# Optimization experiments

Measured on AMD Instinct MI355X. Metric: run time of the kernel, lower is better.

## Reference

```python
import jax, jax.numpy as jnp
import numpy as np

V = 100000   # num nodes
T = 8        # num edge types
E = 400000   # edges per type
D = 128      # node feature dim


def setup_inputs() -> dict:
    key = jax.random.key(0)
    k1, k2, k3 = jax.random.split(key, 3)
    node_values = jax.random.normal(k1, (V, D), dtype=jnp.float32)
    # edges[t, 0] = src indices, edges[t, 1] = dest indices for edge type t
    edges = jax.random.randint(k2, (T, 2, E), 0, V, dtype=jnp.int32)
    W = jax.random.normal(k3, (T * D, D), dtype=jnp.float32) * 0.02
    b = jnp.zeros((D,), dtype=jnp.float32)
    return {"node_values": node_values, "edges": edges, "W": W, "b": b}


def reference(node_values, edges, W, b):
    Vn = node_values.shape[0]

    def per_type(src, dest):
        # norm_weights: sqrt(degree) per node, computed from index occurrence counts
        deg_src = jnp.zeros((Vn,), node_values.dtype).at[src].add(1.0)
        deg_dst = jnp.zeros((Vn,), node_values.dtype).at[dest].add(1.0)
        ns = jnp.sqrt(jnp.maximum(deg_src, 1.0))  # [V]
        nd = jnp.sqrt(jnp.maximum(deg_dst, 1.0))  # [V]
        msg = (node_values / ns[:, None])[src]                      # gather: [E, D]
        agg = jax.ops.segment_sum(msg, dest, num_segments=Vn)       # reduce: [V, D]
        return agg / nd[:, None]

    # vmap over edge types: [T, V, D]
    msgs = jax.vmap(per_type)(edges[:, 0], edges[:, 1])
    # tf.stack(..., axis=1) -> [V, T, D]; reshape to [V, T*D]
    msgs = jnp.transpose(msgs, (1, 0, 2)).reshape(Vn, -1)
    # Dense
    return msgs @ W + b
```

## Files before the change

kernel.cpp:

```cpp
#include <hip/hip_runtime.h>
#include <hip/hip_bf16.h>
#include <stdint.h>

#define NV 100000
#define NT 8
#define NE 400000
#define ND 128
#define NTV (NT * NV)
#define SC1B ((NTV + 1023) / 1024)
#define XCVT ((NV * ND / 8) / 256)

typedef float  f32x4  __attribute__((ext_vector_type(4)));
typedef short  bf16x8 __attribute__((ext_vector_type(8)));

static __device__ __forceinline__ unsigned short f2bf(float f) {
    unsigned u = __float_as_uint(f);
    u += 0x7fffu + ((u >> 16) & 1u);
    return (unsigned short)(u >> 16);
}

__global__ __launch_bounds__(256) void k_count(const int* __restrict__ edges,
                                               unsigned* __restrict__ cs,
                                               unsigned* __restrict__ cd) {
    int i = blockIdx.x * 256 + threadIdx.x;
    if (i >= NT * NE / 4) return;
    int t = i / (NE / 4);
    int e = (i - t * (NE / 4)) * 4;
    const int* base = edges + (size_t)t * 2 * NE;
    int4 s4 = *(const int4*)&base[e];
    int4 d4 = *(const int4*)&base[NE + e];
    unsigned* cst = cs + t * NV;
    unsigned* cdt = cd + t * NV;
    atomicAdd(&cst[s4.x], 1u); atomicAdd(&cst[s4.y], 1u);
    atomicAdd(&cst[s4.z], 1u); atomicAdd(&cst[s4.w], 1u);
    atomicAdd(&cdt[d4.x], 1u); atomicAdd(&cdt[d4.y], 1u);
    atomicAdd(&cdt[d4.z], 1u); atomicAdd(&cdt[d4.w], 1u);
}

__global__ __launch_bounds__(256) void k_scan1(const unsigned* __restrict__ cnt,
                                               unsigned* __restrict__ off,
                                               unsigned* __restrict__ bsum) {
    __shared__ unsigned sm[256];
    int tid  = threadIdx.x;
    int base = blockIdx.x * 1024 + tid * 4;
    unsigned v0 = (base + 0 < NTV) ? cnt[base + 0] : 0u;
    unsigned v1 = (base + 1 < NTV) ? cnt[base + 1] : 0u;
    unsigned v2 = (base + 2 < NTV) ? cnt[base + 2] : 0u;
    unsigned v3 = (base + 3 < NTV) ? cnt[base + 3] : 0u;
    unsigned s4 = v0 + v1 + v2 + v3;
    sm[tid] = s4;
    __syncthreads();
    for (int d = 1; d < 256; d <<= 1) {
        unsigned tv = (tid >= d) ? sm[tid - d] : 0u;
        __syncthreads();
        sm[tid] += tv;
        __syncthreads();
    }
    unsigned excl = sm[tid] - s4;
    if (tid == 255) bsum[blockIdx.x] = sm[255];
    if (base + 0 < NTV) off[base + 0] = excl;
    if (base + 1 < NTV) off[base + 1] = excl + v0;
    if (base + 2 < NTV) off[base + 2] = excl + v0 + v1;
    if (base + 3 < NTV) off[base + 3] = excl + v0 + v1 + v2;
}

__global__ __launch_bounds__(1024) void k_scan2(unsigned* __restrict__ bsum) {
    __shared__ unsigned sm[1024];
    int tid = threadIdx.x;
    unsigned v = (tid < SC1B) ? bsum[tid] : 0u;
    sm[tid] = v;
    __syncthreads();
    for (int d = 1; d < 1024; d <<= 1) {
        unsigned tv = (tid >= d) ? sm[tid - d] : 0u;
        __syncthreads();
        sm[tid] += tv;
        __syncthreads();
    }
    if (tid < SC1B) bsum[tid] = sm[tid] - v;
}

__global__ __launch_bounds__(256) void k_scan3(unsigned* __restrict__ off,
                                               const unsigned* __restrict__ bsum,
                                               unsigned* __restrict__ cursor,
                                               unsigned* __restrict__ cs) {
    int i = blockIdx.x * 256 + threadIdx.x;
    if (i < NTV) {
        unsigned v = off[i] + bsum[i >> 10];
        off[i]    = v;
        cursor[i] = v;
        unsigned a = cs[i];
        ((float*)cs)[i] = rsqrtf((float)(a > 1u ? a : 1u));
    }
    if (i == 0) off[NTV] = (unsigned)(NT * NE);
}

__global__ __launch_bounds__(256) void k_cvt(const float* __restrict__ x,
                                             unsigned short* __restrict__ xb,
                                             const float* __restrict__ W,
                                             unsigned short* __restrict__ Wt) {
    if (blockIdx.x < XCVT) {
        int i = blockIdx.x * 256 + threadIdx.x;
        const float4 a = *(const float4*)&x[(size_t)i * 8];
        const float4 b = *(const float4*)&x[(size_t)i * 8 + 4];
        union { unsigned short us[8]; uint4 v; } pk;
        pk.us[0] = f2bf(a.x); pk.us[1] = f2bf(a.y);
        pk.us[2] = f2bf(a.z); pk.us[3] = f2bf(a.w);
        pk.us[4] = f2bf(b.x); pk.us[5] = f2bf(b.y);
        pk.us[6] = f2bf(b.z); pk.us[7] = f2bf(b.w);
        *(uint4*)&xb[(size_t)i * 8] = pk.v;
    } else {
        int i = (blockIdx.x - XCVT) * 256 + threadIdx.x;
        int t = i >> 14;
        int r = i & 16383;
        int col = r >> 7;
        int k   = r & 127;
        Wt[i] = f2bf(W[((size_t)t * 128 + k) * 128 + col]);
    }
}

__global__ __launch_bounds__(256) void k_fill(const int* __restrict__ edges,
                                              unsigned* __restrict__ cursor,
                                              int* __restrict__ elist) {
    int i = blockIdx.x * 256 + threadIdx.x;
    if (i >= NT * NE / 4) return;
    int t = i / (NE / 4);
    int e = (i - t * (NE / 4)) * 4;
    const int* base = edges + (size_t)t * 2 * NE;
    int4 s4 = *(const int4*)&base[e];
    int4 d4 = *(const int4*)&base[NE + e];
    unsigned* curt = cursor + t * NV;
    unsigned p0 = atomicAdd(&curt[d4.x], 1u); elist[p0] = s4.x;
    unsigned p1 = atomicAdd(&curt[d4.y], 1u); elist[p1] = s4.y;
    unsigned p2 = atomicAdd(&curt[d4.z], 1u); elist[p2] = s4.z;
    unsigned p3 = atomicAdd(&curt[d4.w], 1u); elist[p3] = s4.w;
}

#define ACC8(dst, c, s)                                                      \
    do {                                                                     \
        (dst)[0] = fmaf(__uint_as_float((c).x << 16), (s), (dst)[0]);        \
        (dst)[1] = fmaf(__uint_as_float((c).x & 0xffff0000u), (s), (dst)[1]);\
        (dst)[2] = fmaf(__uint_as_float((c).y << 16), (s), (dst)[2]);        \
        (dst)[3] = fmaf(__uint_as_float((c).y & 0xffff0000u), (s), (dst)[3]);\
        (dst)[4] = fmaf(__uint_as_float((c).z << 16), (s), (dst)[4]);        \
        (dst)[5] = fmaf(__uint_as_float((c).z & 0xffff0000u), (s), (dst)[5]);\
        (dst)[6] = fmaf(__uint_as_float((c).w << 16), (s), (dst)[6]);        \
        (dst)[7] = fmaf(__uint_as_float((c).w & 0xffff0000u), (s), (dst)[7]);\
    } while (0)

__global__ __launch_bounds__(256, 4) void k_fused(
    const unsigned short* __restrict__ xb, const unsigned short* __restrict__ Wt,
    const float* __restrict__ inv_ns, const unsigned* __restrict__ off,
    const int* __restrict__ elist, const float* __restrict__ bias,
    float* __restrict__ out)
{
    const int lane  = threadIdx.x & 63;
    const int wid   = threadIdx.x >> 6;
    const int row0  = blockIdx.x * 64 + wid * 16;
    const int arow  = lane & 15;
    const int g     = lane >> 4;
    const int myrow = row0 + arow;
    const bool rowok = (myrow < NV);
    const int rowi  = rowok ? myrow : 0;

    f32x4 acc[8];
#pragma unroll
    for (int cf = 0; cf < 8; ++cf) acc[cf] = (f32x4){0.f, 0.f, 0.f, 0.f};

    for (int t = 0; t < NT; ++t) {
        float ga[32];
#pragma unroll
        for (int j = 0; j < 32; ++j) ga[j] = 0.f;

        const int ti = t * NV + rowi;
        unsigned e0 = off[ti];
        unsigned e1 = rowok ? off[ti + 1] : e0;
        unsigned dd = e1 - e0;
        float snd = rsqrtf((float)(dd > 1u ? dd : 1u));
        const float* insb = inv_ns + (size_t)t * NV;

        for (unsigned e = e0; e < e1; ++e) {
            int   src = elist[e];
            float sns = insb[src];
            const uint4* xp = (const uint4*)(xb + (size_t)src * ND) + g;
            uint4 c0 = xp[0];
            uint4 c1 = xp[4];
            uint4 c2 = xp[8];
            uint4 c3 = xp[12];
            ACC8(ga + 0,  c0, sns);
            ACC8(ga + 8,  c1, sns);
            ACC8(ga + 16, c2, sns);
            ACC8(ga + 24, c3, sns);
        }

#pragma unroll
        for (int ks = 0; ks < 4; ++ks) {
            union { unsigned short u[8]; bf16x8 v; } af;
#pragma unroll
            for (int j = 0; j < 8; ++j) af.u[j] = f2bf(ga[ks * 8 + j] * snd);
#pragma unroll
            for (int cf = 0; cf < 8; ++cf) {
                const bf16x8 bf = *(const bf16x8*)&Wt[((size_t)(t * 128 + cf * 16 + arow)) * 128 + ks * 32 + g * 8];
                acc[cf] = __builtin_amdgcn_mfma_f32_16x16x32_bf16(af.v, bf, acc[cf], 0, 0, 0);
            }
        }
    }

#pragma unroll
    for (int i2 = 0; i2 < 4; ++i2) {
        int row = row0 + g * 4 + i2;
        if (row < NV) {
#pragma unroll
            for (int cf = 0; cf < 8; ++cf)
                out[(size_t)row * ND + cf * 16 + arow] = acc[cf][i2] + bias[cf * 16 + arow];
        }
    }
}

extern "C" void kernel_launch(void* const* d_in, const int* in_sizes, int n_in,
                              void* d_out, int out_size, void* d_ws, size_t ws_size,
                              hipStream_t stream) {
    const float* x     = (const float*)d_in[0];
    const int*   edges = (const int*)d_in[1];
    const float* W     = (const float*)d_in[2];
    const float* b     = (const float*)d_in[3];
    float*       out   = (float*)d_out;

    unsigned short* xb     = (unsigned short*)d_ws;
    unsigned short* Wt     = xb + (size_t)NV * ND;
    unsigned*       cs     = (unsigned*)(Wt + (size_t)NT * ND * ND);
    unsigned*       cd     = cs + NTV;
    unsigned*       off    = cd + NTV;
    unsigned*       bsum   = off + NTV + 1;
    unsigned*       cursor = bsum + 1024;
    int*            elist  = (int*)(cursor + NTV);

    const size_t need = (size_t)NV * ND * 2 + (size_t)NT * ND * ND * 2 +
                        ((size_t)3 * NTV + (NTV + 1) + 1024) * 4 +
                        (size_t)NT * NE * 4;
    if (ws_size < need) return;

    hipMemsetAsync(cs, 0, (size_t)2 * NTV * sizeof(unsigned), stream);
    k_count<<<(NT * NE / 4 + 255) / 256, 256, 0, stream>>>(edges, cs, cd);
    k_scan1<<<SC1B, 256, 0, stream>>>(cd, off, bsum);
    k_scan2<<<1, 1024, 0, stream>>>(bsum);
    k_scan3<<<(NTV + 255) / 256, 256, 0, stream>>>(off, bsum, cursor, cs);
    k_cvt<<<XCVT + (NT * ND * ND) / 256, 256, 0, stream>>>(x, xb, W, Wt);
    k_fill<<<(NT * NE / 4 + 255) / 256, 256, 0, stream>>>(edges, cursor, elist);
    k_fused<<<(NV + 63) / 64, 256, 0, stream>>>(xb, Wt, (const float*)cs, off, elist, b, out);
}
```

Before: 860.7 us.

## Flatten per-segment edge loop with LDS atomic accumulation and packed edge records

Replaces the per-row serial edge loop with a flattened loop over all edges of a 16-row segment, one edge per lane, accumulating into shared memory via atomic adds with a rotated bank layout. The fill kernel now writes packed records containing source index, local dest row and precomputed source norm, removing a dependent gather. This targets load imbalance from skewed degrees, but adds many LDS atomics, doubles edge-list size and uses 32KB shared memory per block.

```diff
diff --git a/kernel.cpp b/kernel.cpp
--- a/kernel.cpp
+++ b/kernel.cpp
@@ -119,8 +119,9 @@
 }
 
 __global__ __launch_bounds__(256) void k_fill(const int* __restrict__ edges,
+                                              const float* __restrict__ inv_ns,
                                               unsigned* __restrict__ cursor,
-                                              int* __restrict__ elist) {
+                                              uint2* __restrict__ elist2) {
     int i = blockIdx.x * 256 + threadIdx.x;
     if (i >= NT * NE / 4) return;
     int t = i / (NE / 4);
@@ -128,75 +129,93 @@
     const int* base = edges + (size_t)t * 2 * NE;
     int4 s4 = *(const int4*)&base[e];
     int4 d4 = *(const int4*)&base[NE + e];
-    unsigned* curt = cursor + t * NV;
-    unsigned p0 = atomicAdd(&curt[d4.x], 1u); elist[p0] = s4.x;
-    unsigned p1 = atomicAdd(&curt[d4.y], 1u); elist[p1] = s4.y;
-    unsigned p2 = atomicAdd(&curt[d4.z], 1u); elist[p2] = s4.z;
-    unsigned p3 = atomicAdd(&curt[d4.w], 1u); elist[p3] = s4.w;
-}
-
-#define ACC8(dst, c, s)                                                      \
-    do {                                                                     \
-        (dst)[0] = fmaf(__uint_as_float((c).x << 16), (s), (dst)[0]);        \
-        (dst)[1] = fmaf(__uint_as_float((c).x & 0xffff0000u), (s), (dst)[1]);\
-        (dst)[2] = fmaf(__uint_as_float((c).y << 16), (s), (dst)[2]);        \
-        (dst)[3] = fmaf(__uint_as_float((c).y & 0xffff0000u), (s), (dst)[3]);\
-        (dst)[4] = fmaf(__uint_as_float((c).z << 16), (s), (dst)[4]);        \
-        (dst)[5] = fmaf(__uint_as_float((c).z & 0xffff0000u), (s), (dst)[5]);\
-        (dst)[6] = fmaf(__uint_as_float((c).w << 16), (s), (dst)[6]);        \
-        (dst)[7] = fmaf(__uint_as_float((c).w & 0xffff0000u), (s), (dst)[7]);\
-    } while (0)
+    const float* insb = inv_ns + (size_t)t * NV;
+    unsigned*    curt = cursor + t * NV;
+    unsigned p0 = atomicAdd(&curt[d4.x], 1u);
+    elist2[p0] = make_uint2((unsigned)s4.x | (((unsigned)d4.x & 15u) << 17),
+                            __float_as_uint(insb[s4.x]));
+    unsigned p1 = atomicAdd(&curt[d4.y], 1u);
+    elist2[p1] = make_uint2((unsigned)s4.y | (((unsigned)d4.y & 15u) << 17),
+                            __float_as_uint(insb[s4.y]));
+    unsigned p2 = atomicAdd(&curt[d4.z], 1u);
+    elist2[p2] = make_uint2((unsigned)s4.z | (((unsigned)d4.z & 15u) << 17),
+                            __float_as_uint(insb[s4.z]));
+    unsigned p3 = atomicAdd(&curt[d4.w], 1u);
+    elist2[p3] = make_uint2((unsigned)s4.w | (((unsigned)d4.w & 15u) << 17),
+                            __float_as_uint(insb[s4.w]));
+}
+
+static __device__ __forceinline__ void ds_acc2(float* __restrict__ aw, int rot,
+                                               int kb, unsigned cw, float sns) {
+    atomicAdd(&aw[(kb + rot) & 31],     __uint_as_float(cw << 16) * sns);
+    atomicAdd(&aw[(kb + 1 + rot) & 31], __uint_as_float(cw & 0xffff0000u) * sns);
+}
 
 __global__ __launch_bounds__(256, 4) void k_fused(
     const unsigned short* __restrict__ xb, const unsigned short* __restrict__ Wt,
-    const float* __restrict__ inv_ns, const unsigned* __restrict__ off,
-    const int* __restrict__ elist, const float* __restrict__ bias,
-    float* __restrict__ out)
+    const unsigned* __restrict__ off, const uint2* __restrict__ elist2,
+    const float* __restrict__ bias, float* __restrict__ out)
 {
+    __shared__ float agg[4][16][128];
     const int lane  = threadIdx.x & 63;
     const int wid   = threadIdx.x >> 6;
     const int row0  = blockIdx.x * 64 + wid * 16;
     const int arow  = lane & 15;
     const int g     = lane >> 4;
     const int myrow = row0 + arow;
-    const bool rowok = (myrow < NV);
-    const int rowi  = rowok ? myrow : 0;
 
     f32x4 acc[8];
 #pragma unroll
     for (int cf = 0; cf < 8; ++cf) acc[cf] = (f32x4){0.f, 0.f, 0.f, 0.f};
 
+    const int rlo = (row0 < NV) ? row0 : NV;
+    const int rhi = (row0 + 16 < NV) ? row0 + 16 : NV;
+
     for (int t = 0; t < NT; ++t) {
-        float ga[32];
-#pragma unroll
-        for (int j = 0; j < 32; ++j) ga[j] = 0.f;
-
-        const int ti = t * NV + rowi;
-        unsigned e0 = off[ti];
-        unsigned e1 = rowok ? off[ti + 1] : e0;
-        unsigned dd = e1 - e0;
+        float4* z = (float4*)&agg[wid][0][0];
+#pragma unroll
+        for (int it = 0; it < 8; ++it) z[it * 64 + lane] = make_float4(0.f, 0.f, 0.f, 0.f);
+        __asm__ volatile("s_waitcnt lgkmcnt(0)" ::: "memory");
+
+        const unsigned e0 = off[t * NV + rlo];
+        const unsigned e1 = off[t * NV + rhi];
+
+        for (unsigned base = e0; base < e1; base += 16) {
+            unsigned e = base + (unsigned)arow;
+            if (e < e1) {
+                uint2 p   = elist2[e];
+                int   src = (int)(p.x & 0x1FFFFu);
+                int   r   = (int)(p.x >> 17);
+                float sns = __uint_as_float(p.y);
+                const uint4* xp = (const uint4*)(xb + (size_t)src * ND) + g * 4;
+                uint4 c0 = xp[0], c1 = xp[1], c2 = xp[2], c3 = xp[3];
+                float* aw = &agg[wid][r][g * 32];
+                const int rot = (r + 16 * g) & 31;
+                ds_acc2(aw, rot, 0,  c0.x, sns); ds_acc2(aw, rot, 2,  c0.y, sns);
+                ds_acc2(aw, rot, 4,  c0.z, sns); ds_acc2(aw, rot, 6,  c0.w, sns);
+                ds_acc2(aw, rot, 8,  c1.x, sns); ds_acc2(aw, rot, 10, c1.y, sns);
+                ds_acc2(aw, rot, 12, c1.z, sns); ds_acc2(aw, rot, 14, c1.w, sns);
+                ds_acc2(aw, rot, 16, c2.x, sns); ds_acc2(aw, rot, 18, c2.y, sns);
+                ds_acc2(aw, rot, 20, c2.z, sns); ds_acc2(aw, rot, 22, c2.w, sns);
+                ds_acc2(aw, rot, 24, c3.x, sns); ds_acc2(aw, rot, 26, c3.y, sns);
+                ds_acc2(aw, rot, 28, c3.z, sns); ds_acc2(aw, rot, 30, c3.w, sns);
+            }
+        }
+        __asm__ volatile("s_waitcnt lgkmcnt(0)" ::: "memory");
+
+        int ci = t * NV + (myrow < NV ? myrow : NV - 1);
+        unsigned dd = off[ci + 1] - off[ci];
         float snd = rsqrtf((float)(dd > 1u ? dd : 1u));
-        const float* insb = inv_ns + (size_t)t * NV;
-
-        for (unsigned e = e0; e < e1; ++e) {
-            int   src = elist[e];
-            float sns = insb[src];
-            const uint4* xp = (const uint4*)(xb + (size_t)src * ND) + g;
-            uint4 c0 = xp[0];
-            uint4 c1 = xp[4];
-            uint4 c2 = xp[8];
-            uint4 c3 = xp[12];
-            ACC8(ga + 0,  c0, sns);
-            ACC8(ga + 8,  c1, sns);
-            ACC8(ga + 16, c2, sns);
-            ACC8(ga + 24, c3, sns);
-        }
 
 #pragma unroll
         for (int ks = 0; ks < 4; ++ks) {
             union { unsigned short u[8]; bf16x8 v; } af;
-#pragma unroll
-            for (int j = 0; j < 8; ++j) af.u[j] = f2bf(ga[ks * 8 + j] * snd);
+            const int rot2 = (arow + 16 * ks) & 31;
+#pragma unroll
+            for (int j = 0; j < 8; ++j) {
+                float val = agg[wid][arow][ks * 32 + ((g * 8 + j + rot2) & 31)];
+                af.u[j] = f2bf(val * snd);
+            }
 #pragma unroll
             for (int cf = 0; cf < 8; ++cf) {
                 const bf16x8 bf = *(const bf16x8*)&Wt[((size_t)(t * 128 + cf * 16 + arow)) * 128 + ks * 32 + g * 8];
@@ -227,16 +246,16 @@
 
     unsigned short* xb     = (unsigned short*)d_ws;
     unsigned short* Wt     = xb + (size_t)NV * ND;
-    unsigned*       cs     = (unsigned*)(Wt + (size_t)NT * ND * ND);
+    uint2*          elist2 = (uint2*)(Wt + (size_t)NT * ND * ND);
+    unsigned*       cs     = (unsigned*)(elist2 + (size_t)NT * NE);
     unsigned*       cd     = cs + NTV;
     unsigned*       off    = cd + NTV;
     unsigned*       bsum   = off + NTV + 1;
     unsigned*       cursor = bsum + 1024;
-    int*            elist  = (int*)(cursor + NTV);
 
     const size_t need = (size_t)NV * ND * 2 + (size_t)NT * ND * ND * 2 +
-                        ((size_t)3 * NTV + (NTV + 1) + 1024) * 4 +
-                        (size_t)NT * NE * 4;
+                        (size_t)NT * NE * 8 +
+                        ((size_t)3 * NTV + (NTV + 1) + 1024) * 4;
     if (ws_size < need) return;
 
     hipMemsetAsync(cs, 0, (size_t)2 * NTV * sizeof(unsigned), stream);
@@ -245,6 +264,6 @@
     k_scan2<<<1, 1024, 0, stream>>>(bsum);
     k_scan3<<<(NTV + 255) / 256, 256, 0, stream>>>(off, bsum, cursor, cs);
     k_cvt<<<XCVT + (NT * ND * ND) / 256, 256, 0, stream>>>(x, xb, W, Wt);
-    k_fill<<<(NT * NE / 4 + 255) / 256, 256, 0, stream>>>(edges, cursor, elist);
-    k_fused<<<(NV + 63) / 64, 256, 0, stream>>>(xb, Wt, (const float*)cs, off, elist, b, out);
-}
+    k_fill<<<(NT * NE / 4 + 255) / 256, 256, 0, stream>>>(edges, (const float*)cs, cursor, elist2);
+    k_fused<<<(NV + 63) / 64, 256, 0, stream>>>(xb, Wt, off, elist2, b, out);
+}
```

Result: slower. 3.372 ms (+291.8%).
